# Kernel tuning notes

Measured on AMD Instinct MI355X. Metric: run time of the kernel, lower is better.

## Reference

```python
import jax, jax.numpy as jnp
import numpy as np

N = 50000        # num_nodes
E = 1_600_000    # num_edges (before self loops)
IN = 128         # in_channels
C = 16           # out_channels per head
H = 4            # heads
ED = 16          # edge_dim
SLOPE = 0.2      # LeakyReLU negative slope


def setup_inputs() -> dict:
    key = jax.random.key(0)
    ks = jax.random.split(key, 9)
    x = jax.random.normal(ks[0], (N, IN), jnp.float32)
    edge_index = jax.random.randint(ks[1], (2, E), 0, N)
    edge_attr = jax.random.normal(ks[2], (E, ED), jnp.float32)
    # GATConv parameters (PyG layout): node lin (no bias), attention vectors, edge lin
    W = jax.random.normal(ks[3], (IN, H * C), jnp.float32) / np.float32(np.sqrt(IN))
    att_src = jax.random.normal(ks[4], (H, C), jnp.float32) / np.float32(np.sqrt(C))
    att_dst = jax.random.normal(ks[5], (H, C), jnp.float32) / np.float32(np.sqrt(C))
    W_edge = jax.random.normal(ks[6], (ED, H * C), jnp.float32) / np.float32(np.sqrt(ED))
    att_edge = jax.random.normal(ks[7], (H, C), jnp.float32) / np.float32(np.sqrt(C))
    bias = jnp.zeros((H * C,), jnp.float32)
    return {"x": x, "edge_index": edge_index, "edge_attr": edge_attr,
            "W": W, "att_src": att_src, "att_dst": att_dst,
            "W_edge": W_edge, "att_edge": att_edge, "bias": bias}


def reference(x, edge_index, edge_attr, W, att_src, att_dst, W_edge, att_edge, bias):
    num_nodes = x.shape[0]
    # GATLayer: add self loops (PyG fills self-loop edge_attr with 1.0)
    loops = jnp.arange(num_nodes, dtype=edge_index.dtype)
    ei = jnp.concatenate([edge_index, jnp.stack([loops, loops])], axis=1)
    ea = jnp.concatenate(
        [edge_attr, jnp.ones((num_nodes, edge_attr.shape[1]), edge_attr.dtype)], axis=0)
    src, dst = ei[0], ei[1]  # messages flow src -> dst
    # eval mode: feat_dropout / edge_dropout are no-ops
    h = (x @ W).reshape(num_nodes, H, C)              # [N,H,C]
    a_src = jnp.einsum('nhc,hc->nh', h, att_src)       # [N,H]
    a_dst = jnp.einsum('nhc,hc->nh', h, att_dst)       # [N,H]
    e = (ea @ W_edge).reshape(-1, H, C)                # [E',H,C]
    a_e = jnp.einsum('ehc,hc->eh', e, att_edge)        # [E',H]
    alpha = a_src[src] + a_dst[dst] + a_e              # per-edge logits [E',H]
    alpha = jax.nn.leaky_relu(alpha, SLOPE)
    # segment softmax over incoming edges of each dst node (every node has a self loop)
    amax = jax.ops.segment_max(alpha, dst, num_segments=num_nodes)
    ex = jnp.exp(alpha - amax[dst])
    denom = jax.ops.segment_sum(ex, dst, num_segments=num_nodes)
    att = ex / denom[dst]                              # [E',H]
    # scatter-add aggregation of weighted source features
    out = jax.ops.segment_sum(att[:, :, None] * h[src], dst, num_segments=num_nodes)
    return out.reshape(num_nodes, H * C) + bias        # concat heads + bias
```

## Files before the change

kernel.cpp:

```cpp
#include <hip/hip_runtime.h>
#include <hip/hip_bf16.h>
#include <cstdint>

#define IN_CH 128
#define HC    64
#define ED    16
#define SLOPE 0.2f

__device__ __forceinline__ uint32_t f2bf(float x) {
  uint32_t b = __float_as_uint(x);
  return (b + 0x7fffu + ((b >> 16) & 1u)) >> 16;
}
__device__ __forceinline__ float bf2f(uint32_t h) {
  return __uint_as_float(h << 16);
}

__global__ __launch_bounds__(256) void k_node(
    const float* __restrict__ x, const float* __restrict__ W,
    const float* __restrict__ att_src_p, const float* __restrict__ att_dst_p,
    float* __restrict__ h, float* __restrict__ a_src, float* __restrict__ a_dst,
    int N)
{
  int lane = threadIdx.x & 63;
  int gw = (blockIdx.x * blockDim.x + threadIdx.x) >> 6;
  int nwaves = (gridDim.x * blockDim.x) >> 6;
  float asv = att_src_p[lane];
  float adv = att_dst_p[lane];
  for (int n0 = gw * 4; n0 < N; n0 += nwaves * 4) {
    int n1 = min(n0 + 1, N - 1), n2 = min(n0 + 2, N - 1), n3 = min(n0 + 3, N - 1);
    const float4* xa = (const float4*)(x + (size_t)n0 * IN_CH);
    const float4* xb = (const float4*)(x + (size_t)n1 * IN_CH);
    const float4* xc = (const float4*)(x + (size_t)n2 * IN_CH);
    const float4* xd = (const float4*)(x + (size_t)n3 * IN_CH);
    float acc0 = 0.f, acc1 = 0.f, acc2 = 0.f, acc3 = 0.f;
#pragma unroll 4
    for (int k4 = 0; k4 < IN_CH / 4; k4++) {
      float4 va = xa[k4], vb = xb[k4], vc = xc[k4], vd = xd[k4];
      float w0 = W[(k4 * 4 + 0) * HC + lane];
      float w1 = W[(k4 * 4 + 1) * HC + lane];
      float w2 = W[(k4 * 4 + 2) * HC + lane];
      float w3 = W[(k4 * 4 + 3) * HC + lane];
      acc0 += va.x * w0 + va.y * w1 + va.z * w2 + va.w * w3;
      acc1 += vb.x * w0 + vb.y * w1 + vb.z * w2 + vb.w * w3;
      acc2 += vc.x * w0 + vc.y * w1 + vc.z * w2 + vc.w * w3;
      acc3 += vd.x * w0 + vd.y * w1 + vd.z * w2 + vd.w * w3;
    }
    h[(size_t)n0 * HC + lane] = acc0;
    if (n0 + 1 < N) h[(size_t)n1 * HC + lane] = acc1;
    if (n0 + 2 < N) h[(size_t)n2 * HC + lane] = acc2;
    if (n0 + 3 < N) h[(size_t)n3 * HC + lane] = acc3;
    float s0 = acc0 * asv, s1 = acc1 * asv, s2 = acc2 * asv, s3 = acc3 * asv;
    float d0 = acc0 * adv, d1 = acc1 * adv, d2 = acc2 * adv, d3 = acc3 * adv;
#pragma unroll
    for (int m = 1; m < 16; m <<= 1) {
      s0 += __shfl_xor(s0, m); s1 += __shfl_xor(s1, m);
      s2 += __shfl_xor(s2, m); s3 += __shfl_xor(s3, m);
      d0 += __shfl_xor(d0, m); d1 += __shfl_xor(d1, m);
      d2 += __shfl_xor(d2, m); d3 += __shfl_xor(d3, m);
    }
    if ((lane & 15) == 0) {
      int hh = lane >> 4;
      a_src[(size_t)n0 * 4 + hh] = s0; a_dst[(size_t)n0 * 4 + hh] = d0;
      if (n0 + 1 < N) { a_src[(size_t)n1 * 4 + hh] = s1; a_dst[(size_t)n1 * 4 + hh] = d1; }
      if (n0 + 2 < N) { a_src[(size_t)n2 * 4 + hh] = s2; a_dst[(size_t)n2 * 4 + hh] = d2; }
      if (n0 + 3 < N) { a_src[(size_t)n3 * 4 + hh] = s3; a_dst[(size_t)n3 * 4 + hh] = d3; }
    }
  }
}

__global__ __launch_bounds__(256) void k_hist(const int* __restrict__ dst, int E,
                                              int* __restrict__ deg)
{
  int e = blockIdx.x * 256 + threadIdx.x;
  if (e < E) atomicAdd(&deg[dst[e]], 1);
}

__global__ __launch_bounds__(256) void k_scan_a(const int* __restrict__ deg, int N,
                                                int* __restrict__ rowptr,
                                                int* __restrict__ blksums)
{
  __shared__ int tsum[256];
  int tid = threadIdx.x;
  int base = blockIdx.x * 2048 + tid * 8;
  int pre[8];
  int s = 0;
#pragma unroll
  for (int j = 0; j < 8; j++) {
    int idx = base + j;
    int v = (idx < N) ? deg[idx] : 0;
    pre[j] = s; s += v;
  }
  tsum[tid] = s;
  __syncthreads();
  for (int offm = 1; offm < 256; offm <<= 1) {
    int t = (tid >= offm) ? tsum[tid - offm] : 0;
    __syncthreads();
    tsum[tid] += t;
    __syncthreads();
  }
  int excl = tsum[tid] - s;
#pragma unroll
  for (int j = 0; j < 8; j++) {
    int idx = base + j;
    if (idx < N) rowptr[idx] = excl + pre[j];
  }
  if (tid == 255) blksums[blockIdx.x] = tsum[255];
}

__global__ void k_scan_b(int* __restrict__ blksums, int NB)
{
  if (threadIdx.x == 0 && blockIdx.x == 0) {
    int run = 0;
    for (int b = 0; b < NB; b++) { int t = blksums[b]; blksums[b] = run; run += t; }
  }
}

__global__ __launch_bounds__(256) void k_scan_c(int* __restrict__ rowptr,
                                                const int* __restrict__ blksums,
                                                int N, int E)
{
  int i = blockIdx.x * 256 + threadIdx.x;
  if (i < N) rowptr[i] += blksums[i >> 11];
  if (i == 0) rowptr[N] = E;
}

__global__ __launch_bounds__(256) void k_edge3(
    const int* __restrict__ ei, const float* __restrict__ ea,
    const float* __restrict__ W_edge, const float* __restrict__ att_edge,
    const float* __restrict__ a_src, const float* __restrict__ a_dst,
    const int* __restrict__ rowptr, int* __restrict__ cursor,
    uint4* __restrict__ pay, int E)
{
  __shared__ float ve[ED * 4];
  if (threadIdx.x < 64) {
    int d = threadIdx.x >> 2, hh = threadIdx.x & 3;
    float s = 0.f;
#pragma unroll
    for (int c = 0; c < 16; c++) s += W_edge[d * HC + hh * 16 + c] * att_edge[hh * 16 + c];
    ve[d * 4 + hh] = s;
  }
  __syncthreads();
  int e = blockIdx.x * 256 + threadIdx.x;
  if (e >= E) return;
  int sn = ei[e], dn = ei[E + e];
  float4 as4 = *(const float4*)(a_src + (size_t)sn * 4);
  float4 ad4 = *(const float4*)(a_dst + (size_t)dn * 4);
  const float4* ea4 = (const float4*)(ea + (size_t)e * ED);
  float4 q0 = ea4[0], q1 = ea4[1], q2 = ea4[2], q3 = ea4[3];
  float eav[16] = {q0.x,q0.y,q0.z,q0.w, q1.x,q1.y,q1.z,q1.w,
                   q2.x,q2.y,q2.z,q2.w, q3.x,q3.y,q3.z,q3.w};
  float ae0 = 0.f, ae1 = 0.f, ae2 = 0.f, ae3 = 0.f;
#pragma unroll
  for (int d = 0; d < ED; d++) {
    float v = eav[d];
    ae0 += v * ve[d * 4 + 0]; ae1 += v * ve[d * 4 + 1];
    ae2 += v * ve[d * 4 + 2]; ae3 += v * ve[d * 4 + 3];
  }
  float al0 = as4.x + ad4.x + ae0;
  float al1 = as4.y + ad4.y + ae1;
  float al2 = as4.z + ad4.z + ae2;
  float al3 = as4.w + ad4.w + ae3;
  al0 = al0 > 0.f ? al0 : SLOPE * al0;
  al1 = al1 > 0.f ? al1 : SLOPE * al1;
  al2 = al2 > 0.f ? al2 : SLOPE * al2;
  al3 = al3 > 0.f ? al3 : SLOPE * al3;
  int pos = rowptr[dn] + atomicAdd(&cursor[dn], 1);
  uint4 r;
  r.x = (uint32_t)sn;
  r.y = f2bf(__expf(al0)) | (f2bf(__expf(al1)) << 16);
  r.z = f2bf(__expf(al2)) | (f2bf(__expf(al3)) << 16);
  r.w = 0u;
  pay[pos] = r;
}

__global__ __launch_bounds__(256) void k_agg3(
    const float* __restrict__ h,
    const float* __restrict__ a_src, const float* __restrict__ a_dst,
    const float* __restrict__ W_edge, const float* __restrict__ att_edge,
    const float* __restrict__ bias, const int* __restrict__ rowptr,
    const uint4* __restrict__ pay, float* __restrict__ out, int N)
{
  __shared__ float aes[4];
  if (threadIdx.x < 4) {
    int hh = threadIdx.x;
    float s = 0.f;
    for (int d = 0; d < ED; d++) {
      float vd = 0.f;
#pragma unroll
      for (int c = 0; c < 16; c++) vd += W_edge[d * HC + hh * 16 + c] * att_edge[hh * 16 + c];
      s += vd;
    }
    aes[hh] = s;
  }
  __syncthreads();
  int lane = threadIdx.x & 63;
  int n = blockIdx.x * 4 + (threadIdx.x >> 6);
  if (n >= N) return;
  int hq = lane >> 4;
  int b = rowptr[n], e = rowptr[n + 1];
  float acc = 0.f, den = 0.f;
  int p = b;
  for (; p + 3 < e; p += 4) {
    uint4 r0 = pay[p], r1 = pay[p + 1], r2 = pay[p + 2], r3 = pay[p + 3];
    uint32_t w0 = (hq & 2) ? r0.z : r0.y;
    uint32_t w1 = (hq & 2) ? r1.z : r1.y;
    uint32_t w2 = (hq & 2) ? r2.z : r2.y;
    uint32_t w3 = (hq & 2) ? r3.z : r3.y;
    float e0 = bf2f((hq & 1) ? (w0 >> 16) : (w0 & 0xffffu));
    float e1 = bf2f((hq & 1) ? (w1 >> 16) : (w1 & 0xffffu));
    float e2 = bf2f((hq & 1) ? (w2 >> 16) : (w2 & 0xffffu));
    float e3 = bf2f((hq & 1) ? (w3 >> 16) : (w3 & 0xffffu));
    float h0 = h[(size_t)r0.x * HC + lane];
    float h1 = h[(size_t)r1.x * HC + lane];
    float h2 = h[(size_t)r2.x * HC + lane];
    float h3 = h[(size_t)r3.x * HC + lane];
    acc += e0 * h0 + e1 * h1 + e2 * h2 + e3 * h3;
    den += (e0 + e1) + (e2 + e3);
  }
  for (; p < e; p++) {
    uint4 r0 = pay[p];
    uint32_t w0 = (hq & 2) ? r0.z : r0.y;
    float e0 = bf2f((hq & 1) ? (w0 >> 16) : (w0 & 0xffffu));
    acc += e0 * h[(size_t)r0.x * HC + lane];
    den += e0;
  }
  float al = a_src[(size_t)n * 4 + hq] + a_dst[(size_t)n * 4 + hq] + aes[hq];
  al = al > 0.f ? al : SLOPE * al;
  float exs = __expf(al);
  acc += exs * h[(size_t)n * HC + lane];
  den += exs;
  out[(size_t)n * HC + lane] = acc / den + bias[lane];
}

extern "C" void kernel_launch(void* const* d_in, const int* in_sizes, int n_in,
                              void* d_out, int out_size, void* d_ws, size_t ws_size,
                              hipStream_t stream)
{
  const float* x        = (const float*)d_in[0];
  const int*   ei       = (const int*)d_in[1];
  const float* ea       = (const float*)d_in[2];
  const float* W        = (const float*)d_in[3];
  const float* att_src  = (const float*)d_in[4];
  const float* att_dst  = (const float*)d_in[5];
  const float* W_edge   = (const float*)d_in[6];
  const float* att_edge = (const float*)d_in[7];
  const float* bias     = (const float*)d_in[8];
  float* out = (float*)d_out;

  int N = in_sizes[0] / IN_CH;
  int E = in_sizes[1] / 2;

  uint8_t* ws = (uint8_t*)d_ws;
  size_t off = 0;
  auto alloc = [&](size_t bytes) -> void* {
    void* p = ws + off;
    off = (off + bytes + 255) & ~(size_t)255;
    return p;
  };
  float* h        = (float*)alloc((size_t)N * HC * 4);
  float* a_src_w  = (float*)alloc((size_t)N * 4 * 4);
  float* a_dst_w  = (float*)alloc((size_t)N * 4 * 4);
  int*   deg      = (int*)alloc((size_t)N * 2 * 4);
  int*   cursor   = deg + N;
  int*   rowptr   = (int*)alloc(((size_t)N + 1) * 4);
  int*   blksums  = (int*)alloc(64 * 4);
  uint4* pay      = (uint4*)alloc((size_t)E * 16);
  (void)ws_size; (void)n_in; (void)out_size;

  hipMemsetAsync(deg, 0, (size_t)N * 2 * 4, stream);

  k_node<<<512, 256, 0, stream>>>(x, W, att_src, att_dst, h, a_src_w, a_dst_w, N);
  k_hist<<<(E + 255) / 256, 256, 0, stream>>>(ei + E, E, deg);
  int NB = (N + 2047) / 2048;
  k_scan_a<<<NB, 256, 0, stream>>>(deg, N, rowptr, blksums);
  k_scan_b<<<1, 64, 0, stream>>>(blksums, NB);
  k_scan_c<<<(N + 255) / 256, 256, 0, stream>>>(rowptr, blksums, N, E);
  k_edge3<<<(E + 255) / 256, 256, 0, stream>>>(ei, ea, W_edge, att_edge,
                                               a_src_w, a_dst_w, rowptr, cursor,
                                               pay, E);
  k_agg3<<<(N + 3) / 4, 256, 0, stream>>>(h, a_src_w, a_dst_w, W_edge, att_edge,
                                          bias, rowptr, pay, out, N);
}
```

Before: 506.6 us.

## Merge scan kernels, seed cursor with rowptr, batch edges per thread

The three-kernel scan becomes one single-block 1024-thread scan that also seeds the cursor array with row offsets, so the edge kernel no longer reads rowptr. The histogram handles four destinations per thread with an int4 load, and the edge kernel handles two edges per thread. The node kernel now launches one block per 16 nodes instead of using a grid-stride loop, and the aggregation loop unroll goes from 4 to 8 to keep more gathers in flight. The single-block scan walks about 49 elements serially per thread and may be slow, and the extra unrolling raises register pressure.

```diff
diff --git a/kernel.cpp b/kernel.cpp
--- a/kernel.cpp
+++ b/kernel.cpp
@@ -22,114 +22,101 @@
     int N)
 {
   int lane = threadIdx.x & 63;
-  int gw = (blockIdx.x * blockDim.x + threadIdx.x) >> 6;
-  int nwaves = (gridDim.x * blockDim.x) >> 6;
+  int wv = threadIdx.x >> 6;
   float asv = att_src_p[lane];
   float adv = att_dst_p[lane];
-  for (int n0 = gw * 4; n0 < N; n0 += nwaves * 4) {
-    int n1 = min(n0 + 1, N - 1), n2 = min(n0 + 2, N - 1), n3 = min(n0 + 3, N - 1);
-    const float4* xa = (const float4*)(x + (size_t)n0 * IN_CH);
-    const float4* xb = (const float4*)(x + (size_t)n1 * IN_CH);
-    const float4* xc = (const float4*)(x + (size_t)n2 * IN_CH);
-    const float4* xd = (const float4*)(x + (size_t)n3 * IN_CH);
-    float acc0 = 0.f, acc1 = 0.f, acc2 = 0.f, acc3 = 0.f;
+  int n0 = (blockIdx.x * 4 + wv) * 4;
+  if (n0 >= N) return;
+  int n1 = min(n0 + 1, N - 1), n2 = min(n0 + 2, N - 1), n3 = min(n0 + 3, N - 1);
+  const float4* xa = (const float4*)(x + (size_t)n0 * IN_CH);
+  const float4* xb = (const float4*)(x + (size_t)n1 * IN_CH);
+  const float4* xc = (const float4*)(x + (size_t)n2 * IN_CH);
+  const float4* xd = (const float4*)(x + (size_t)n3 * IN_CH);
+  float acc0 = 0.f, acc1 = 0.f, acc2 = 0.f, acc3 = 0.f;
 #pragma unroll 4
-    for (int k4 = 0; k4 < IN_CH / 4; k4++) {
-      float4 va = xa[k4], vb = xb[k4], vc = xc[k4], vd = xd[k4];
-      float w0 = W[(k4 * 4 + 0) * HC + lane];
-      float w1 = W[(k4 * 4 + 1) * HC + lane];
-      float w2 = W[(k4 * 4 + 2) * HC + lane];
-      float w3 = W[(k4 * 4 + 3) * HC + lane];
-      acc0 += va.x * w0 + va.y * w1 + va.z * w2 + va.w * w3;
-      acc1 += vb.x * w0 + vb.y * w1 + vb.z * w2 + vb.w * w3;
-      acc2 += vc.x * w0 + vc.y * w1 + vc.z * w2 + vc.w * w3;
-      acc3 += vd.x * w0 + vd.y * w1 + vd.z * w2 + vd.w * w3;
-    }
-    h[(size_t)n0 * HC + lane] = acc0;
-    if (n0 + 1 < N) h[(size_t)n1 * HC + lane] = acc1;
-    if (n0 + 2 < N) h[(size_t)n2 * HC + lane] = acc2;
-    if (n0 + 3 < N) h[(size_t)n3 * HC + lane] = acc3;
-    float s0 = acc0 * asv, s1 = acc1 * asv, s2 = acc2 * asv, s3 = acc3 * asv;
-    float d0 = acc0 * adv, d1 = acc1 * adv, d2 = acc2 * adv, d3 = acc3 * adv;
+  for (int k4 = 0; k4 < IN_CH / 4; k4++) {
+    float4 va = xa[k4], vb = xb[k4], vc = xc[k4], vd = xd[k4];
+    float w0 = W[(k4 * 4 + 0) * HC + lane];
+    float w1 = W[(k4 * 4 + 1) * HC + lane];
+    float w2 = W[(k4 * 4 + 2) * HC + lane];
+    float w3 = W[(k4 * 4 + 3) * HC + lane];
+    acc0 += va.x * w0 + va.y * w1 + va.z * w2 + va.w * w3;
+    acc1 += vb.x * w0 + vb.y * w1 + vb.z * w2 + vb.w * w3;
+    acc2 += vc.x * w0 + vc.y * w1 + vc.z * w2 + vc.w * w3;
+    acc3 += vd.x * w0 + vd.y * w1 + vd.z * w2 + vd.w * w3;
+  }
+  h[(size_t)n0 * HC + lane] = acc0;
+  if (n0 + 1 < N) h[(size_t)n1 * HC + lane] = acc1;
+  if (n0 + 2 < N) h[(size_t)n2 * HC + lane] = acc2;
+  if (n0 + 3 < N) h[(size_t)n3 * HC + lane] = acc3;
+  float s0 = acc0 * asv, s1 = acc1 * asv, s2 = acc2 * asv, s3 = acc3 * asv;
+  float d0 = acc0 * adv, d1 = acc1 * adv, d2 = acc2 * adv, d3 = acc3 * adv;
 #pragma unroll
-    for (int m = 1; m < 16; m <<= 1) {
-      s0 += __shfl_xor(s0, m); s1 += __shfl_xor(s1, m);
-      s2 += __shfl_xor(s2, m); s3 += __shfl_xor(s3, m);
-      d0 += __shfl_xor(d0, m); d1 += __shfl_xor(d1, m);
-      d2 += __shfl_xor(d2, m); d3 += __shfl_xor(d3, m);
-    }
-    if ((lane & 15) == 0) {
-      int hh = lane >> 4;
-      a_src[(size_t)n0 * 4 + hh] = s0; a_dst[(size_t)n0 * 4 + hh] = d0;
-      if (n0 + 1 < N) { a_src[(size_t)n1 * 4 + hh] = s1; a_dst[(size_t)n1 * 4 + hh] = d1; }
-      if (n0 + 2 < N) { a_src[(size_t)n2 * 4 + hh] = s2; a_dst[(size_t)n2 * 4 + hh] = d2; }
-      if (n0 + 3 < N) { a_src[(size_t)n3 * 4 + hh] = s3; a_dst[(size_t)n3 * 4 + hh] = d3; }
-    }
+  for (int m = 1; m < 16; m <<= 1) {
+    s0 += __shfl_xor(s0, m); s1 += __shfl_xor(s1, m);
+    s2 += __shfl_xor(s2, m); s3 += __shfl_xor(s3, m);
+    d0 += __shfl_xor(d0, m); d1 += __shfl_xor(d1, m);
+    d2 += __shfl_xor(d2, m); d3 += __shfl_xor(d3, m);
+  }
+  if ((lane & 15) == 0) {
+    int hh = lane >> 4;
+    a_src[(size_t)n0 * 4 + hh] = s0; a_dst[(size_t)n0 * 4 + hh] = d0;
+    if (n0 + 1 < N) { a_src[(size_t)n1 * 4 + hh] = s1; a_dst[(size_t)n1 * 4 + hh] = d1; }
+    if (n0 + 2 < N) { a_src[(size_t)n2 * 4 + hh] = s2; a_dst[(size_t)n2 * 4 + hh] = d2; }
+    if (n0 + 3 < N) { a_src[(size_t)n3 * 4 + hh] = s3; a_dst[(size_t)n3 * 4 + hh] = d3; }
   }
 }
 
 __global__ __launch_bounds__(256) void k_hist(const int* __restrict__ dst, int E,
                                               int* __restrict__ deg)
 {
-  int e = blockIdx.x * 256 + threadIdx.x;
-  if (e < E) atomicAdd(&deg[dst[e]], 1);
-}
-
-__global__ __launch_bounds__(256) void k_scan_a(const int* __restrict__ deg, int N,
+  int t = blockIdx.x * 256 + threadIdx.x;
+  int e0 = t * 4;
+  if (e0 + 3 < E) {
+    int4 d4 = *(const int4*)(dst + e0);
+    atomicAdd(&deg[d4.x], 1);
+    atomicAdd(&deg[d4.y], 1);
+    atomicAdd(&deg[d4.z], 1);
+    atomicAdd(&deg[d4.w], 1);
+  } else {
+    for (int e = e0; e < E; e++) atomicAdd(&deg[dst[e]], 1);
+  }
+}
+
+__global__ __launch_bounds__(1024) void k_scan1(const int* __restrict__ deg,
+                                                int N, int E,
                                                 int* __restrict__ rowptr,
-                                                int* __restrict__ blksums)
-{
-  __shared__ int tsum[256];
+                                                int* __restrict__ cursor)
+{
+  __shared__ int ts[1024];
   int tid = threadIdx.x;
-  int base = blockIdx.x * 2048 + tid * 8;
-  int pre[8];
+  int M = (N + 1023) >> 10;
+  int lo = tid * M;
+  int hi = min(lo + M, N);
   int s = 0;
-#pragma unroll
-  for (int j = 0; j < 8; j++) {
-    int idx = base + j;
-    int v = (idx < N) ? deg[idx] : 0;
-    pre[j] = s; s += v;
-  }
-  tsum[tid] = s;
+  for (int i = lo; i < hi; i++) s += deg[i];
+  ts[tid] = s;
   __syncthreads();
-  for (int offm = 1; offm < 256; offm <<= 1) {
-    int t = (tid >= offm) ? tsum[tid - offm] : 0;
+  for (int o = 1; o < 1024; o <<= 1) {
+    int v = (tid >= o) ? ts[tid - o] : 0;
     __syncthreads();
-    tsum[tid] += t;
+    ts[tid] += v;
     __syncthreads();
   }
-  int excl = tsum[tid] - s;
-#pragma unroll
-  for (int j = 0; j < 8; j++) {
-    int idx = base + j;
-    if (idx < N) rowptr[idx] = excl + pre[j];
-  }
-  if (tid == 255) blksums[blockIdx.x] = tsum[255];
-}
-
-__global__ void k_scan_b(int* __restrict__ blksums, int NB)
-{
-  if (threadIdx.x == 0 && blockIdx.x == 0) {
-    int run = 0;
-    for (int b = 0; b < NB; b++) { int t = blksums[b]; blksums[b] = run; run += t; }
-  }
-}
-
-__global__ __launch_bounds__(256) void k_scan_c(int* __restrict__ rowptr,
-                                                const int* __restrict__ blksums,
-                                                int N, int E)
-{
-  int i = blockIdx.x * 256 + threadIdx.x;
-  if (i < N) rowptr[i] += blksums[i >> 11];
-  if (i == 0) rowptr[N] = E;
+  int run = ts[tid] - s;
+  for (int i = lo; i < hi; i++) {
+    rowptr[i] = run;
+    cursor[i] = run;
+    run += deg[i];
+  }
+  if (tid == 1023) rowptr[N] = E;
 }
 
 __global__ __launch_bounds__(256) void k_edge3(
     const int* __restrict__ ei, const float* __restrict__ ea,
     const float* __restrict__ W_edge, const float* __restrict__ att_edge,
     const float* __restrict__ a_src, const float* __restrict__ a_dst,
-    const int* __restrict__ rowptr, int* __restrict__ cursor,
-    uint4* __restrict__ pay, int E)
+    int* __restrict__ cursor, uint4* __restrict__ pay, int E)
 {
   __shared__ float ve[ED * 4];
   if (threadIdx.x < 64) {
@@ -140,37 +127,58 @@
     ve[d * 4 + hh] = s;
   }
   __syncthreads();
-  int e = blockIdx.x * 256 + threadIdx.x;
-  if (e >= E) return;
-  int sn = ei[e], dn = ei[E + e];
-  float4 as4 = *(const float4*)(a_src + (size_t)sn * 4);
-  float4 ad4 = *(const float4*)(a_dst + (size_t)dn * 4);
-  const float4* ea4 = (const float4*)(ea + (size_t)e * ED);
-  float4 q0 = ea4[0], q1 = ea4[1], q2 = ea4[2], q3 = ea4[3];
-  float eav[16] = {q0.x,q0.y,q0.z,q0.w, q1.x,q1.y,q1.z,q1.w,
+  int t = blockIdx.x * 256 + threadIdx.x;
+  int e0 = t * 2;
+  if (e0 >= E) return;
+  int e1 = e0 + 1;
+  bool has1 = (e1 < E);
+  int sn0 = ei[e0], dn0 = ei[E + e0];
+  int sn1 = has1 ? ei[e1] : sn0;
+  int dn1 = has1 ? ei[E + e1] : dn0;
+  float4 as0 = *(const float4*)(a_src + (size_t)sn0 * 4);
+  float4 as1 = *(const float4*)(a_src + (size_t)sn1 * 4);
+  float4 ad0 = *(const float4*)(a_dst + (size_t)dn0 * 4);
+  float4 ad1 = *(const float4*)(a_dst + (size_t)dn1 * 4);
+  const float4* ea0 = (const float4*)(ea + (size_t)e0 * ED);
+  const float4* ea1 = (const float4*)(ea + (size_t)e1 * ED);
+  float4 p0 = ea0[0], p1 = ea0[1], p2 = ea0[2], p3 = ea0[3];
+  float4 q0 = has1 ? ea1[0] : p0, q1 = has1 ? ea1[1] : p1;
+  float4 q2 = has1 ? ea1[2] : p2, q3 = has1 ? ea1[3] : p3;
+  float ev0[16] = {p0.x,p0.y,p0.z,p0.w, p1.x,p1.y,p1.z,p1.w,
+                   p2.x,p2.y,p2.z,p2.w, p3.x,p3.y,p3.z,p3.w};
+  float ev1[16] = {q0.x,q0.y,q0.z,q0.w, q1.x,q1.y,q1.z,q1.w,
                    q2.x,q2.y,q2.z,q2.w, q3.x,q3.y,q3.z,q3.w};
-  float ae0 = 0.f, ae1 = 0.f, ae2 = 0.f, ae3 = 0.f;
+  float a00 = 0.f, a01 = 0.f, a02 = 0.f, a03 = 0.f;
+  float a10 = 0.f, a11 = 0.f, a12 = 0.f, a13 = 0.f;
 #pragma unroll
   for (int d = 0; d < ED; d++) {
-    float v = eav[d];
-    ae0 += v * ve[d * 4 + 0]; ae1 += v * ve[d * 4 + 1];
-    ae2 += v * ve[d * 4 + 2]; ae3 += v * ve[d * 4 + 3];
-  }
-  float al0 = as4.x + ad4.x + ae0;
-  float al1 = as4.y + ad4.y + ae1;
-  float al2 = as4.z + ad4.z + ae2;
-  float al3 = as4.w + ad4.w + ae3;
-  al0 = al0 > 0.f ? al0 : SLOPE * al0;
-  al1 = al1 > 0.f ? al1 : SLOPE * al1;
-  al2 = al2 > 0.f ? al2 : SLOPE * al2;
-  al3 = al3 > 0.f ? al3 : SLOPE * al3;
-  int pos = rowptr[dn] + atomicAdd(&cursor[dn], 1);
-  uint4 r;
-  r.x = (uint32_t)sn;
-  r.y = f2bf(__expf(al0)) | (f2bf(__expf(al1)) << 16);
-  r.z = f2bf(__expf(al2)) | (f2bf(__expf(al3)) << 16);
-  r.w = 0u;
-  pay[pos] = r;
+    float v0 = ev0[d], v1 = ev1[d];
+    a00 += v0 * ve[d * 4 + 0]; a01 += v0 * ve[d * 4 + 1];
+    a02 += v0 * ve[d * 4 + 2]; a03 += v0 * ve[d * 4 + 3];
+    a10 += v1 * ve[d * 4 + 0]; a11 += v1 * ve[d * 4 + 1];
+    a12 += v1 * ve[d * 4 + 2]; a13 += v1 * ve[d * 4 + 3];
+  }
+  float l00 = as0.x + ad0.x + a00, l01 = as0.y + ad0.y + a01;
+  float l02 = as0.z + ad0.z + a02, l03 = as0.w + ad0.w + a03;
+  float l10 = as1.x + ad1.x + a10, l11 = as1.y + ad1.y + a11;
+  float l12 = as1.z + ad1.z + a12, l13 = as1.w + ad1.w + a13;
+  l00 = l00 > 0.f ? l00 : SLOPE * l00;  l01 = l01 > 0.f ? l01 : SLOPE * l01;
+  l02 = l02 > 0.f ? l02 : SLOPE * l02;  l03 = l03 > 0.f ? l03 : SLOPE * l03;
+  l10 = l10 > 0.f ? l10 : SLOPE * l10;  l11 = l11 > 0.f ? l11 : SLOPE * l11;
+  l12 = l12 > 0.f ? l12 : SLOPE * l12;  l13 = l13 > 0.f ? l13 : SLOPE * l13;
+  int pos0 = atomicAdd(&cursor[dn0], 1);
+  int pos1 = has1 ? atomicAdd(&cursor[dn1], 1) : 0;
+  uint4 r0, r1;
+  r0.x = (uint32_t)sn0;
+  r0.y = f2bf(__expf(l00)) | (f2bf(__expf(l01)) << 16);
+  r0.z = f2bf(__expf(l02)) | (f2bf(__expf(l03)) << 16);
+  r0.w = 0u;
+  r1.x = (uint32_t)sn1;
+  r1.y = f2bf(__expf(l10)) | (f2bf(__expf(l11)) << 16);
+  r1.z = f2bf(__expf(l12)) | (f2bf(__expf(l13)) << 16);
+  r1.w = 0u;
+  pay[pos0] = r0;
+  if (has1) pay[pos1] = r1;
 }
 
 __global__ __launch_bounds__(256) void k_agg3(
@@ -200,22 +208,36 @@
   int b = rowptr[n], e = rowptr[n + 1];
   float acc = 0.f, den = 0.f;
   int p = b;
-  for (; p + 3 < e; p += 4) {
-    uint4 r0 = pay[p], r1 = pay[p + 1], r2 = pay[p + 2], r3 = pay[p + 3];
+  for (; p + 7 < e; p += 8) {
+    uint4 r0 = pay[p],     r1 = pay[p + 1], r2 = pay[p + 2], r3 = pay[p + 3];
+    uint4 r4 = pay[p + 4], r5 = pay[p + 5], r6 = pay[p + 6], r7 = pay[p + 7];
     uint32_t w0 = (hq & 2) ? r0.z : r0.y;
     uint32_t w1 = (hq & 2) ? r1.z : r1.y;
     uint32_t w2 = (hq & 2) ? r2.z : r2.y;
     uint32_t w3 = (hq & 2) ? r3.z : r3.y;
+    uint32_t w4 = (hq & 2) ? r4.z : r4.y;
+    uint32_t w5 = (hq & 2) ? r5.z : r5.y;
+    uint32_t w6 = (hq & 2) ? r6.z : r6.y;
+    uint32_t w7 = (hq & 2) ? r7.z : r7.y;
     float e0 = bf2f((hq & 1) ? (w0 >> 16) : (w0 & 0xffffu));
     float e1 = bf2f((hq & 1) ? (w1 >> 16) : (w1 & 0xffffu));
     float e2 = bf2f((hq & 1) ? (w2 >> 16) : (w2 & 0xffffu));
     float e3 = bf2f((hq & 1) ? (w3 >> 16) : (w3 & 0xffffu));
+    float e4 = bf2f((hq & 1) ? (w4 >> 16) : (w4 & 0xffffu));
+    float e5 = bf2f((hq & 1) ? (w5 >> 16) : (w5 & 0xffffu));
+    float e6 = bf2f((hq & 1) ? (w6 >> 16) : (w6 & 0xffffu));
+    float e7 = bf2f((hq & 1) ? (w7 >> 16) : (w7 & 0xffffu));
     float h0 = h[(size_t)r0.x * HC + lane];
     float h1 = h[(size_t)r1.x * HC + lane];
     float h2 = h[(size_t)r2.x * HC + lane];
     float h3 = h[(size_t)r3.x * HC + lane];
+    float h4 = h[(size_t)r4.x * HC + lane];
+    float h5 = h[(size_t)r5.x * HC + lane];
+    float h6 = h[(size_t)r6.x * HC + lane];
+    float h7 = h[(size_t)r7.x * HC + lane];
     acc += e0 * h0 + e1 * h1 + e2 * h2 + e3 * h3;
-    den += (e0 + e1) + (e2 + e3);
+    acc += e4 * h4 + e5 * h5 + e6 * h6 + e7 * h7;
+    den += (e0 + e1) + (e2 + e3) + (e4 + e5) + (e6 + e7);
   }
   for (; p < e; p++) {
     uint4 r0 = pay[p];
@@ -260,24 +282,21 @@
   float* h        = (float*)alloc((size_t)N * HC * 4);
   float* a_src_w  = (float*)alloc((size_t)N * 4 * 4);
   float* a_dst_w  = (float*)alloc((size_t)N * 4 * 4);
-  int*   deg      = (int*)alloc((size_t)N * 2 * 4);
-  int*   cursor   = deg + N;
+  int*   deg      = (int*)alloc((size_t)N * 4);
+  int*   cursor   = (int*)alloc((size_t)N * 4);
   int*   rowptr   = (int*)alloc(((size_t)N + 1) * 4);
-  int*   blksums  = (int*)alloc(64 * 4);
   uint4* pay      = (uint4*)alloc((size_t)E * 16);
   (void)ws_size; (void)n_in; (void)out_size;
 
-  hipMemsetAsync(deg, 0, (size_t)N * 2 * 4, stream);
-
-  k_node<<<512, 256, 0, stream>>>(x, W, att_src, att_dst, h, a_src_w, a_dst_w, N);
-  k_hist<<<(E + 255) / 256, 256, 0, stream>>>(ei + E, E, deg);
-  int NB = (N + 2047) / 2048;
-  k_scan_a<<<NB, 256, 0, stream>>>(deg, N, rowptr, blksums);
-  k_scan_b<<<1, 64, 0, stream>>>(blksums, NB);
-  k_scan_c<<<(N + 255) / 256, 256, 0, stream>>>(rowptr, blksums, N, E);
-  k_edge3<<<(E + 255) / 256, 256, 0, stream>>>(ei, ea, W_edge, att_edge,
-                                               a_src_w, a_dst_w, rowptr, cursor,
-                                               pay, E);
+  hipMemsetAsync(deg, 0, (size_t)N * 4, stream);
+
+  k_node<<<(N + 15) / 16, 256, 0, stream>>>(x, W, att_src, att_dst,
+                                            h, a_src_w, a_dst_w, N);
+  k_hist<<<(E / 4 + 255) / 256, 256, 0, stream>>>(ei + E, E, deg);
+  k_scan1<<<1, 1024, 0, stream>>>(deg, N, E, rowptr, cursor);
+  k_edge3<<<(E / 2 + 255) / 256, 256, 0, stream>>>(ei, ea, W_edge, att_edge,
+                                                   a_src_w, a_dst_w, cursor,
+                                                   pay, E);
   k_agg3<<<(N + 3) / 4, 256, 0, stream>>>(h, a_src_w, a_dst_w, W_edge, att_edge,
                                           bias, rowptr, pay, out, N);
 }
```

New measurement: 623.5 us. +23.1%, slower.

## Launch one wave per node quad, vectorize histogram, prefill cursors, unroll aggregation

Applied to the files above, without the earlier changes.

k_node drops its grid-stride loop and launches one wave per group of four nodes, so many more blocks run. k_hist reads four dst indices per thread with one int4 load. k_scan_c now seeds the cursor array with row offsets, so k_edge3 drops its extra rowptr gather and gets the slot straight from the atomic. k_agg3 unrolls its gather loop to eight edges to put more loads in flight, at the cost of more registers.

```diff
diff --git a/kernel.cpp b/kernel.cpp
--- a/kernel.cpp
+++ b/kernel.cpp
@@ -22,57 +22,65 @@
     int N)
 {
   int lane = threadIdx.x & 63;
-  int gw = (blockIdx.x * blockDim.x + threadIdx.x) >> 6;
-  int nwaves = (gridDim.x * blockDim.x) >> 6;
+  int wv = threadIdx.x >> 6;
   float asv = att_src_p[lane];
   float adv = att_dst_p[lane];
-  for (int n0 = gw * 4; n0 < N; n0 += nwaves * 4) {
-    int n1 = min(n0 + 1, N - 1), n2 = min(n0 + 2, N - 1), n3 = min(n0 + 3, N - 1);
-    const float4* xa = (const float4*)(x + (size_t)n0 * IN_CH);
-    const float4* xb = (const float4*)(x + (size_t)n1 * IN_CH);
-    const float4* xc = (const float4*)(x + (size_t)n2 * IN_CH);
-    const float4* xd = (const float4*)(x + (size_t)n3 * IN_CH);
-    float acc0 = 0.f, acc1 = 0.f, acc2 = 0.f, acc3 = 0.f;
+  int n0 = (blockIdx.x * 4 + wv) * 4;
+  if (n0 >= N) return;
+  int n1 = min(n0 + 1, N - 1), n2 = min(n0 + 2, N - 1), n3 = min(n0 + 3, N - 1);
+  const float4* xa = (const float4*)(x + (size_t)n0 * IN_CH);
+  const float4* xb = (const float4*)(x + (size_t)n1 * IN_CH);
+  const float4* xc = (const float4*)(x + (size_t)n2 * IN_CH);
+  const float4* xd = (const float4*)(x + (size_t)n3 * IN_CH);
+  float acc0 = 0.f, acc1 = 0.f, acc2 = 0.f, acc3 = 0.f;
 #pragma unroll 4
-    for (int k4 = 0; k4 < IN_CH / 4; k4++) {
-      float4 va = xa[k4], vb = xb[k4], vc = xc[k4], vd = xd[k4];
-      float w0 = W[(k4 * 4 + 0) * HC + lane];
-      float w1 = W[(k4 * 4 + 1) * HC + lane];
-      float w2 = W[(k4 * 4 + 2) * HC + lane];
-      float w3 = W[(k4 * 4 + 3) * HC + lane];
-      acc0 += va.x * w0 + va.y * w1 + va.z * w2 + va.w * w3;
-      acc1 += vb.x * w0 + vb.y * w1 + vb.z * w2 + vb.w * w3;
-      acc2 += vc.x * w0 + vc.y * w1 + vc.z * w2 + vc.w * w3;
-      acc3 += vd.x * w0 + vd.y * w1 + vd.z * w2 + vd.w * w3;
-    }
-    h[(size_t)n0 * HC + lane] = acc0;
-    if (n0 + 1 < N) h[(size_t)n1 * HC + lane] = acc1;
-    if (n0 + 2 < N) h[(size_t)n2 * HC + lane] = acc2;
-    if (n0 + 3 < N) h[(size_t)n3 * HC + lane] = acc3;
-    float s0 = acc0 * asv, s1 = acc1 * asv, s2 = acc2 * asv, s3 = acc3 * asv;
-    float d0 = acc0 * adv, d1 = acc1 * adv, d2 = acc2 * adv, d3 = acc3 * adv;
-#pragma unroll
-    for (int m = 1; m < 16; m <<= 1) {
-      s0 += __shfl_xor(s0, m); s1 += __shfl_xor(s1, m);
-      s2 += __shfl_xor(s2, m); s3 += __shfl_xor(s3, m);
-      d0 += __shfl_xor(d0, m); d1 += __shfl_xor(d1, m);
-      d2 += __shfl_xor(d2, m); d3 += __shfl_xor(d3, m);
-    }
-    if ((lane & 15) == 0) {
-      int hh = lane >> 4;
-      a_src[(size_t)n0 * 4 + hh] = s0; a_dst[(size_t)n0 * 4 + hh] = d0;
-      if (n0 + 1 < N) { a_src[(size_t)n1 * 4 + hh] = s1; a_dst[(size_t)n1 * 4 + hh] = d1; }
-      if (n0 + 2 < N) { a_src[(size_t)n2 * 4 + hh] = s2; a_dst[(size_t)n2 * 4 + hh] = d2; }
-      if (n0 + 3 < N) { a_src[(size_t)n3 * 4 + hh] = s3; a_dst[(size_t)n3 * 4 + hh] = d3; }
-    }
+  for (int k4 = 0; k4 < IN_CH / 4; k4++) {
+    float4 va = xa[k4], vb = xb[k4], vc = xc[k4], vd = xd[k4];
+    float w0 = W[(k4 * 4 + 0) * HC + lane];
+    float w1 = W[(k4 * 4 + 1) * HC + lane];
+    float w2 = W[(k4 * 4 + 2) * HC + lane];
+    float w3 = W[(k4 * 4 + 3) * HC + lane];
+    acc0 += va.x * w0 + va.y * w1 + va.z * w2 + va.w * w3;
+    acc1 += vb.x * w0 + vb.y * w1 + vb.z * w2 + vb.w * w3;
+    acc2 += vc.x * w0 + vc.y * w1 + vc.z * w2 + vc.w * w3;
+    acc3 += vd.x * w0 + vd.y * w1 + vd.z * w2 + vd.w * w3;
+  }
+  h[(size_t)n0 * HC + lane] = acc0;
+  if (n0 + 1 < N) h[(size_t)n1 * HC + lane] = acc1;
+  if (n0 + 2 < N) h[(size_t)n2 * HC + lane] = acc2;
+  if (n0 + 3 < N) h[(size_t)n3 * HC + lane] = acc3;
+  float s0 = acc0 * asv, s1 = acc1 * asv, s2 = acc2 * asv, s3 = acc3 * asv;
+  float d0 = acc0 * adv, d1 = acc1 * adv, d2 = acc2 * adv, d3 = acc3 * adv;
+#pragma unroll
+  for (int m = 1; m < 16; m <<= 1) {
+    s0 += __shfl_xor(s0, m); s1 += __shfl_xor(s1, m);
+    s2 += __shfl_xor(s2, m); s3 += __shfl_xor(s3, m);
+    d0 += __shfl_xor(d0, m); d1 += __shfl_xor(d1, m);
+    d2 += __shfl_xor(d2, m); d3 += __shfl_xor(d3, m);
+  }
+  if ((lane & 15) == 0) {
+    int hh = lane >> 4;
+    a_src[(size_t)n0 * 4 + hh] = s0; a_dst[(size_t)n0 * 4 + hh] = d0;
+    if (n0 + 1 < N) { a_src[(size_t)n1 * 4 + hh] = s1; a_dst[(size_t)n1 * 4 + hh] = d1; }
+    if (n0 + 2 < N) { a_src[(size_t)n2 * 4 + hh] = s2; a_dst[(size_t)n2 * 4 + hh] = d2; }
+    if (n0 + 3 < N) { a_src[(size_t)n3 * 4 + hh] = s3; a_dst[(size_t)n3 * 4 + hh] = d3; }
   }
 }
 
 __global__ __launch_bounds__(256) void k_hist(const int* __restrict__ dst, int E,
                                               int* __restrict__ deg)
 {
-  int e = blockIdx.x * 256 + threadIdx.x;
-  if (e < E) atomicAdd(&deg[dst[e]], 1);
+  int t = blockIdx.x * 256 + threadIdx.x;
+  int e0 = t * 4;
+  if (e0 + 3 < E) {
+    int4 d4 = *(const int4*)(dst + e0);
+    atomicAdd(&deg[d4.x], 1);
+    atomicAdd(&deg[d4.y], 1);
+    atomicAdd(&deg[d4.z], 1);
+    atomicAdd(&deg[d4.w], 1);
+  } else {
+    for (int e = e0; e < E; e++) atomicAdd(&deg[dst[e]], 1);
+  }
 }
 
 __global__ __launch_bounds__(256) void k_scan_a(const int* __restrict__ deg, int N,
@@ -116,11 +124,16 @@
 }
 
 __global__ __launch_bounds__(256) void k_scan_c(int* __restrict__ rowptr,
+                                                int* __restrict__ cursor,
                                                 const int* __restrict__ blksums,
                                                 int N, int E)
 {
   int i = blockIdx.x * 256 + threadIdx.x;
-  if (i < N) rowptr[i] += blksums[i >> 11];
+  if (i < N) {
+    int v = rowptr[i] + blksums[i >> 11];
+    rowptr[i] = v;
+    cursor[i] = v;
+  }
   if (i == 0) rowptr[N] = E;
 }
 
@@ -128,8 +141,7 @@
     const int* __restrict__ ei, const float* __restrict__ ea,
     const float* __restrict__ W_edge, const float* __restrict__ att_edge,
     const float* __restrict__ a_src, const float* __restrict__ a_dst,
-    const int* __restrict__ rowptr, int* __restrict__ cursor,
-    uint4* __restrict__ pay, int E)
+    int* __restrict__ cursor, uint4* __restrict__ pay, int E)
 {
   __shared__ float ve[ED * 4];
   if (threadIdx.x < 64) {
@@ -164,7 +176,7 @@
   al1 = al1 > 0.f ? al1 : SLOPE * al1;
   al2 = al2 > 0.f ? al2 : SLOPE * al2;
   al3 = al3 > 0.f ? al3 : SLOPE * al3;
-  int pos = rowptr[dn] + atomicAdd(&cursor[dn], 1);
+  int pos = atomicAdd(&cursor[dn], 1);
   uint4 r;
   r.x = (uint32_t)sn;
   r.y = f2bf(__expf(al0)) | (f2bf(__expf(al1)) << 16);
@@ -200,22 +212,36 @@
   int b = rowptr[n], e = rowptr[n + 1];
   float acc = 0.f, den = 0.f;
   int p = b;
-  for (; p + 3 < e; p += 4) {
-    uint4 r0 = pay[p], r1 = pay[p + 1], r2 = pay[p + 2], r3 = pay[p + 3];
+  for (; p + 7 < e; p += 8) {
+    uint4 r0 = pay[p],     r1 = pay[p + 1], r2 = pay[p + 2], r3 = pay[p + 3];
+    uint4 r4 = pay[p + 4], r5 = pay[p + 5], r6 = pay[p + 6], r7 = pay[p + 7];
     uint32_t w0 = (hq & 2) ? r0.z : r0.y;
     uint32_t w1 = (hq & 2) ? r1.z : r1.y;
     uint32_t w2 = (hq & 2) ? r2.z : r2.y;
     uint32_t w3 = (hq & 2) ? r3.z : r3.y;
+    uint32_t w4 = (hq & 2) ? r4.z : r4.y;
+    uint32_t w5 = (hq & 2) ? r5.z : r5.y;
+    uint32_t w6 = (hq & 2) ? r6.z : r6.y;
+    uint32_t w7 = (hq & 2) ? r7.z : r7.y;
     float e0 = bf2f((hq & 1) ? (w0 >> 16) : (w0 & 0xffffu));
     float e1 = bf2f((hq & 1) ? (w1 >> 16) : (w1 & 0xffffu));
     float e2 = bf2f((hq & 1) ? (w2 >> 16) : (w2 & 0xffffu));
     float e3 = bf2f((hq & 1) ? (w3 >> 16) : (w3 & 0xffffu));
+    float e4 = bf2f((hq & 1) ? (w4 >> 16) : (w4 & 0xffffu));
+    float e5 = bf2f((hq & 1) ? (w5 >> 16) : (w5 & 0xffffu));
+    float e6 = bf2f((hq & 1) ? (w6 >> 16) : (w6 & 0xffffu));
+    float e7 = bf2f((hq & 1) ? (w7 >> 16) : (w7 & 0xffffu));
     float h0 = h[(size_t)r0.x * HC + lane];
     float h1 = h[(size_t)r1.x * HC + lane];
     float h2 = h[(size_t)r2.x * HC + lane];
     float h3 = h[(size_t)r3.x * HC + lane];
+    float h4 = h[(size_t)r4.x * HC + lane];
+    float h5 = h[(size_t)r5.x * HC + lane];
+    float h6 = h[(size_t)r6.x * HC + lane];
+    float h7 = h[(size_t)r7.x * HC + lane];
     acc += e0 * h0 + e1 * h1 + e2 * h2 + e3 * h3;
-    den += (e0 + e1) + (e2 + e3);
+    acc += e4 * h4 + e5 * h5 + e6 * h6 + e7 * h7;
+    den += (e0 + e1) + (e2 + e3) + (e4 + e5) + (e6 + e7);
   }
   for (; p < e; p++) {
     uint4 r0 = pay[p];
@@ -260,23 +286,24 @@
   float* h        = (float*)alloc((size_t)N * HC * 4);
   float* a_src_w  = (float*)alloc((size_t)N * 4 * 4);
   float* a_dst_w  = (float*)alloc((size_t)N * 4 * 4);
-  int*   deg      = (int*)alloc((size_t)N * 2 * 4);
-  int*   cursor   = deg + N;
+  int*   deg      = (int*)alloc((size_t)N * 4);
+  int*   cursor   = (int*)alloc((size_t)N * 4);
   int*   rowptr   = (int*)alloc(((size_t)N + 1) * 4);
   int*   blksums  = (int*)alloc(64 * 4);
   uint4* pay      = (uint4*)alloc((size_t)E * 16);
   (void)ws_size; (void)n_in; (void)out_size;
 
-  hipMemsetAsync(deg, 0, (size_t)N * 2 * 4, stream);
-
-  k_node<<<512, 256, 0, stream>>>(x, W, att_src, att_dst, h, a_src_w, a_dst_w, N);
-  k_hist<<<(E + 255) / 256, 256, 0, stream>>>(ei + E, E, deg);
-  int NB = (N + 2047) / 2048;
-  k_scan_a<<<NB, 256, 0, stream>>>(deg, N, rowptr, blksums);
-  k_scan_b<<<1, 64, 0, stream>>>(blksums, NB);
-  k_scan_c<<<(N + 255) / 256, 256, 0, stream>>>(rowptr, blksums, N, E);
+  hipMemsetAsync(deg, 0, (size_t)N * 4, stream);
+
+  k_node<<<(N + 15) / 16, 256, 0, stream>>>(x, W, att_src, att_dst,
+                                            h, a_src_w, a_dst_w, N);
+  k_hist<<<(E / 4 + 255) / 256, 256, 0, stream>>>(ei + E, E, deg);
+  int NBs = (N + 2047) / 2048;
+  k_scan_a<<<NBs, 256, 0, stream>>>(deg, N, rowptr, blksums);
+  k_scan_b<<<1, 64, 0, stream>>>(blksums, NBs);
+  k_scan_c<<<(N + 255) / 256, 256, 0, stream>>>(rowptr, cursor, blksums, N, E);
   k_edge3<<<(E + 255) / 256, 256, 0, stream>>>(ei, ea, W_edge, att_edge,
-                                               a_src_w, a_dst_w, rowptr, cursor,
+                                               a_src_w, a_dst_w, cursor,
                                                pay, E);
   k_agg3<<<(N + 3) / 4, 256, 0, stream>>>(h, a_src_w, a_dst_w, W_edge, att_edge,
                                           bias, rowptr, pay, out, N);
```

Result: faster. 491.4 us (-3.0%).
